# Performance work log

Measured on AMD Instinct MI355X. Metric: run time of the kernel, lower is better.

The kernel has to match this reference:

```python
import jax, jax.numpy as jnp
import numpy as np

N_NODES = 1_000_000
N_EDGES = 32_000_000

def setup_inputs() -> dict:
    key = jax.random.key(0)
    ks = jax.random.split(key, 10)
    s = lambda fan_in: 1.0 / np.sqrt(fan_in)
    return {
        "node_features": jax.random.normal(ks[0], (N_NODES, 2), dtype=jnp.float32),
        "edge_index": jax.random.randint(ks[1], (2, N_EDGES), 0, N_NODES, dtype=jnp.int64) if jax.config.jax_enable_x64 else jax.random.randint(ks[1], (2, N_EDGES), 0, N_NODES, dtype=jnp.int32),
        "W_msg": jax.random.normal(ks[2], (16, 2), dtype=jnp.float32) * s(2),
        "b_msg": jax.random.normal(ks[3], (16,), dtype=jnp.float32) * s(2),
        "W_ih": jax.random.normal(ks[4], (48, 16), dtype=jnp.float32) * s(16),
        "W_hh": jax.random.normal(ks[5], (48, 16), dtype=jnp.float32) * s(16),
        "b_ih": jax.random.normal(ks[6], (48,), dtype=jnp.float32) * s(16),
        "b_hh": jax.random.normal(ks[7], (48,), dtype=jnp.float32) * s(16),
        "W_cls": jax.random.normal(ks[8], (2, 16), dtype=jnp.float32) * s(16),
        "b_cls": jax.random.normal(ks[9], (2,), dtype=jnp.float32) * s(16),
    }

def reference(node_features, edge_index, W_msg, b_msg, W_ih, W_hh, b_ih, b_hh, W_cls, b_cls):
    N = node_features.shape[0]
    src, dst = edge_index[0], edge_index[1]
    # segment-mean of predecessor features (predecessors of dst are src)
    sums = jax.ops.segment_sum(node_features[src], dst, num_segments=N)  # [N,2]
    cnt = jax.ops.segment_sum(jnp.ones(src.shape, node_features.dtype), dst, num_segments=N)  # [N]
    has_pred = cnt > 0
    agg = jnp.where(has_pred[:, None], sums / jnp.maximum(cnt, 1.0)[:, None], node_features)
    # msg linear: [N,16]
    x = agg @ W_msg.T + b_msg
    # single-step GRU with h0 = 0 (torch nn.GRU gate math)
    h0 = jnp.zeros_like(x)
    gi = x @ W_ih.T + b_ih   # [N,48]
    gh = h0 @ W_hh.T + b_hh  # [N,48]
    i_r, i_z, i_n = jnp.split(gi, 3, axis=-1)
    h_r, h_z, h_n = jnp.split(gh, 3, axis=-1)
    r = jax.nn.sigmoid(i_r + h_r)
    z = jax.nn.sigmoid(i_z + h_z)
    n = jnp.tanh(i_n + r * h_n)
    h = (1.0 - z) * n + z * h0
    # classifier: [N,2]
    return h @ W_cls.T + b_cls
```

## Files before the change

### kernel.cpp

```cpp
#include <hip/hip_runtime.h>


#define NBKT        256
#define BKT_SHIFT   12
#define DLOW_MASK   4095u
#define BKT_CAP     139264u
#define CHUNK       16384
#define BIN_THREADS 512
#define CHUNK2      8192
#define SLICES2     ((BKT_CAP + CHUNK2 - 1) / CHUNK2)
#define ACC_THREADS 1024
#define SPLIT       2
#define BKT_RANGE   4096
#define NODE_SPACE  (NBKT * BKT_RANGE)

__device__ __forceinline__ unsigned long long expand_pkt(unsigned p20)
{
    return (1ull << 52) | ((unsigned long long)(p20 >> 10) << 26)
                        | (unsigned long long)(p20 & 1023u);
}

__global__ __launch_bounds__(256) void tgnn_prep_kernel(
    const float* __restrict__ W_msg, const float* __restrict__ b_msg,
    const float* __restrict__ W_ih,  const float* __restrict__ b_ih,
    const float* __restrict__ b_hh,  const float* __restrict__ W_cls,
    const float* __restrict__ b_cls, float* __restrict__ P,
    unsigned* __restrict__ cursor1, unsigned* __restrict__ cursor2)
{
    int j = threadIdx.x;
    cursor1[j] = (unsigned)j * BKT_CAP;
    cursor2[j] = (unsigned)j * BKT_CAP;
    if (j < 48) {
        float a0 = 0.f, a1 = 0.f, dd = 0.f;
        #pragma unroll
        for (int k = 0; k < 16; ++k) {
            float w = W_ih[j * 16 + k];
            a0 += w * W_msg[k * 2 + 0];
            a1 += w * W_msg[k * 2 + 1];
            dd += w * b_msg[k];
        }
        dd += b_ih[j];
        P[j]      = a0;
        P[48 + j] = a1;
        if (j < 16)      P[96 + j]         = dd + b_hh[j];
        else if (j < 32) P[112 + (j - 16)] = dd + b_hh[j];
        else             P[128 + (j - 32)] = dd;
    }
    if (j < 16) {
        P[144 + j] = b_hh[32 + j];
        P[160 + j] = W_cls[j];
        P[176 + j] = W_cls[16 + j];
    }
    if (j == 0) { P[192] = b_cls[0]; P[193] = b_cls[1]; }
}

__global__ __launch_bounds__(256) void tgnn_quant_kernel(
    const float2* __restrict__ nf, unsigned* __restrict__ qnf, int n)
{
    int i = blockIdx.x * blockDim.x + threadIdx.x;
    if (i >= n) return;
    float2 f = nf[i];
    float x = fminf(fmaxf(f.x, -7.9f), 7.9f);
    float y = fminf(fmaxf(f.y, -7.9f), 7.9f);
    unsigned qx = (unsigned)fmaf(x, 64.0f, 512.5f);
    unsigned qy = (unsigned)fmaf(y, 64.0f, 512.5f);
    qnf[i] = qx | (qy << 10);
}

__global__ __launch_bounds__(BIN_THREADS) void tgnn_bin1_kernel(
    const int* __restrict__ src, const int* __restrict__ dst,
    const unsigned* __restrict__ qnf,
    unsigned* __restrict__ rec1, unsigned* __restrict__ cursor1,
    unsigned long long* __restrict__ partial0,
    int n_edges)
{
    __shared__ unsigned cnt[NBKT];
    __shared__ unsigned pos[NBKT];
    __shared__ unsigned scur[NBKT];
    __shared__ unsigned gbase[NBKT];
    __shared__ unsigned stage[CHUNK];

    int t  = threadIdx.x;
    int e0 = blockIdx.x * CHUNK;
    int ne = n_edges - e0;
    if (ne <= 0) return;
    if (ne > CHUNK) ne = CHUNK;
    int nv4 = (ne + 3) >> 2;

    const int4* s4p = (const int4*)(src + e0);
    const int4* d4p = (const int4*)(dst + e0);

    int4 dr[8], sr[8];
    #pragma unroll
    for (int j = 0; j < 8; ++j) {
        int i4 = j * BIN_THREADS + t;
        if (i4 < nv4) { dr[j] = d4p[i4]; sr[j] = s4p[i4]; }
        else { dr[j] = make_int4(0,0,0,0); sr[j] = make_int4(0,0,0,0); }
    }

    if (t < NBKT) cnt[t] = 0;
    __syncthreads();

    #pragma unroll
    for (int j = 0; j < 8; ++j) {
        int base = 4 * (j * BIN_THREADS + t);
        if (base < ne) {
            int lim = ne - base;
            int sv[4] = { sr[j].x, sr[j].y, sr[j].z, sr[j].w };
            #pragma unroll
            for (int c = 0; c < 4; ++c)
                if (c < lim) atomicAdd(&cnt[((unsigned)sv[c]) >> BKT_SHIFT], 1u);
        }
    }
    __syncthreads();

    if (t < NBKT) pos[t] = cnt[t];
    __syncthreads();
    #pragma unroll
    for (int off = 1; off < NBKT; off <<= 1) {
        unsigned v = 0, a = 0;
        if (t < NBKT) { v = pos[t]; a = (t >= off) ? pos[t - off] : 0u; }
        __syncthreads();
        if (t < NBKT) pos[t] = v + a;
        __syncthreads();
    }
    if (t < NBKT) {
        unsigned myCnt  = cnt[t];
        unsigned myBase = pos[t] - myCnt;
        scur[t] = myBase;
        pos[t]  = myBase;
        gbase[t] = myCnt ? atomicAdd(&cursor1[t], myCnt) : 0u;
    }
    __syncthreads();

    #pragma unroll
    for (int j = 0; j < 8; ++j) {
        int base = 4 * (j * BIN_THREADS + t);
        if (base < ne) {
            int lim = ne - base;
            int sv[4] = { sr[j].x, sr[j].y, sr[j].z, sr[j].w };
            int dv[4] = { dr[j].x, dr[j].y, dr[j].z, dr[j].w };
            #pragma unroll
            for (int c = 0; c < 4; ++c) if (c < lim) {
                unsigned s = (unsigned)sv[c];
                unsigned b = s >> BKT_SHIFT;
                unsigned p = atomicAdd(&scur[b], 1u);
                stage[p] = ((unsigned)dv[c] << 12) | (s & DLOW_MASK);
            }
        }
    }
    __syncthreads();

    int wave = t >> 6, lane = t & 63;
    for (int b = wave; b < NBKT; b += BIN_THREADS / 64) {
        unsigned n = cnt[b];
        if (!n) continue;
        unsigned sb = pos[b];
        unsigned gb = gbase[b];
        unsigned capEnd = (unsigned)(b + 1) * BKT_CAP;
        for (unsigned i = lane; i < n; i += 64) {
            unsigned r = stage[sb + i];
            unsigned slot = gb + i;
            if (slot < capEnd) {
                rec1[slot] = r;
            } else {
                unsigned node = r >> 12;
                unsigned s    = ((unsigned)b << BKT_SHIFT) | (r & DLOW_MASK);
                atomicAdd(&partial0[node], expand_pkt(qnf[s]));
            }
        }
    }
}

__global__ __launch_bounds__(256) void tgnn_pass2_kernel(
    const unsigned* __restrict__ rec1, const unsigned* __restrict__ cursor1,
    const unsigned* __restrict__ qnf,
    unsigned* __restrict__ rec2, unsigned* __restrict__ cursor2,
    unsigned long long* __restrict__ partial0)
{
    __shared__ unsigned qlds[BKT_RANGE];
    __shared__ unsigned cnt[NBKT];
    __shared__ unsigned pos[NBKT];
    __shared__ unsigned scur[NBKT];
    __shared__ unsigned gbase[NBKT];
    __shared__ unsigned stage[CHUNK2];

    int b = blockIdx.y;
    int t = threadIdx.x;

    unsigned count = cursor1[b] - (unsigned)b * BKT_CAP;
    if (count > BKT_CAP) count = BKT_CAP;
    unsigned i0 = (unsigned)blockIdx.x * CHUNK2;
    if (i0 >= count) return;
    unsigned ne = count - i0;
    if (ne > CHUNK2) ne = CHUNK2;
    int nv4 = (int)((ne + 3) >> 2);

    const unsigned* qsrc = qnf + (size_t)b * BKT_RANGE;
    #pragma unroll
    for (int k = 0; k < BKT_RANGE / 256; ++k)
        qlds[k * 256 + t] = qsrc[k * 256 + t];

    const int4* r4p = (const int4*)(rec1 + (size_t)b * BKT_CAP + i0);
    int4 rr[8];
    #pragma unroll
    for (int j = 0; j < 8; ++j) {
        int i4 = j * 256 + t;
        rr[j] = (i4 < nv4) ? r4p[i4] : make_int4(0, 0, 0, 0);
    }

    cnt[t] = 0;
    __syncthreads();

    #pragma unroll
    for (int j = 0; j < 8; ++j) {
        int base = 4 * (j * 256 + t);
        if (base < (int)ne) {
            int lim = (int)ne - base;
            unsigned rv[4] = { (unsigned)rr[j].x, (unsigned)rr[j].y,
                               (unsigned)rr[j].z, (unsigned)rr[j].w };
            #pragma unroll
            for (int c = 0; c < 4; ++c)
                if (c < lim) atomicAdd(&cnt[rv[c] >> 24], 1u);
        }
    }
    __syncthreads();

    pos[t] = cnt[t];
    __syncthreads();
    #pragma unroll
    for (int off = 1; off < NBKT; off <<= 1) {
        unsigned v = pos[t];
        unsigned a = (t >= off) ? pos[t - off] : 0u;
        __syncthreads();
        pos[t] = v + a;
        __syncthreads();
    }
    {
        unsigned myCnt  = cnt[t];
        unsigned myBase = pos[t] - myCnt;
        scur[t] = myBase;
        pos[t]  = myBase;
        gbase[t] = myCnt ? atomicAdd(&cursor2[t], myCnt) : 0u;
    }
    __syncthreads();

    #pragma unroll
    for (int j = 0; j < 8; ++j) {
        int base = 4 * (j * 256 + t);
        if (base < (int)ne) {
            int lim = (int)ne - base;
            unsigned rv[4] = { (unsigned)rr[j].x, (unsigned)rr[j].y,
                               (unsigned)rr[j].z, (unsigned)rr[j].w };
            #pragma unroll
            for (int c = 0; c < 4; ++c) if (c < lim) {
                unsigned r  = rv[c];
                unsigned bb = r >> 24;
                unsigned p  = atomicAdd(&scur[bb], 1u);
                stage[p] = (qlds[r & DLOW_MASK] << 12) | ((r >> 12) & DLOW_MASK);
            }
        }
    }
    __syncthreads();

    int wave = t >> 6, lane = t & 63;
    for (int bb = wave; bb < NBKT; bb += 4) {
        unsigned n = cnt[bb];
        if (!n) continue;
        unsigned sb = pos[bb];
        unsigned gb = gbase[bb];
        unsigned capEnd = (unsigned)(bb + 1) * BKT_CAP;
        for (unsigned i = lane; i < n; i += 64) {
            unsigned r = stage[sb + i];
            unsigned slot = gb + i;
            if (slot < capEnd) {
                rec2[slot] = r;
            } else {
                unsigned node = ((unsigned)bb << BKT_SHIFT) | (r & DLOW_MASK);
                atomicAdd(&partial0[node], expand_pkt(r >> 12));
            }
        }
    }
}

__global__ __launch_bounds__(ACC_THREADS) void tgnn_accum_kernel(
    const unsigned* __restrict__ rec2,
    const unsigned* __restrict__ cursor2,
    unsigned long long* __restrict__ partial)
{
    __shared__ unsigned long long acc[BKT_RANGE];
    int b = blockIdx.x >> 1;
    int s = blockIdx.x & 1;
    int t = threadIdx.x;

    unsigned count = cursor2[b] - (unsigned)b * BKT_CAP;
    if (count > BKT_CAP) count = BKT_CAP;
    unsigned mid = (count >> 1) & ~3u;
    unsigned i0 = s ? mid : 0u;
    unsigned i1 = s ? count : mid;

    unsigned long long* pb = partial + (size_t)s * NODE_SPACE + (size_t)b * BKT_RANGE;
    if (s == 0) {
        #pragma unroll
        for (int k = 0; k < BKT_RANGE / ACC_THREADS; ++k)
            acc[k * ACC_THREADS + t] = pb[k * ACC_THREADS + t];
    } else {
        #pragma unroll
        for (int k = 0; k < BKT_RANGE / ACC_THREADS; ++k)
            acc[k * ACC_THREADS + t] = 0ull;
    }
    __syncthreads();

    const unsigned* rb  = rec2 + (size_t)b * BKT_CAP;
    const int4*     rb4 = (const int4*)rb;

    unsigned v0 = i0 >> 2;
    unsigned v1 = i1 >> 2;
    for (unsigned v = v0 + t; v < v1; v += ACC_THREADS) {
        int4 ra = rb4[v];
        unsigned r0 = (unsigned)ra.x, r1 = (unsigned)ra.y;
        unsigned r2 = (unsigned)ra.z, r3 = (unsigned)ra.w;
        atomicAdd(&acc[r0 & DLOW_MASK], expand_pkt(r0 >> 12));
        atomicAdd(&acc[r1 & DLOW_MASK], expand_pkt(r1 >> 12));
        atomicAdd(&acc[r2 & DLOW_MASK], expand_pkt(r2 >> 12));
        atomicAdd(&acc[r3 & DLOW_MASK], expand_pkt(r3 >> 12));
    }
    for (unsigned i = (v1 << 2) + t; i < i1; i += ACC_THREADS) {
        unsigned r = rb[i];
        atomicAdd(&acc[r & DLOW_MASK], expand_pkt(r >> 12));
    }
    __syncthreads();

    #pragma unroll
    for (int k = 0; k < BKT_RANGE / ACC_THREADS; ++k)
        pb[k * ACC_THREADS + t] = acc[k * ACC_THREADS + t];
}

__global__ __launch_bounds__(256) void tgnn_merge_node_kernel(
    const float2* __restrict__ nf,
    const unsigned long long* __restrict__ partial,
    const float* __restrict__ P,
    float2* __restrict__ out, int n_nodes)
{
    __shared__ float p[194];
    for (int k = threadIdx.x; k < 194; k += 256) p[k] = P[k];
    __syncthreads();

    int i = blockIdx.x * 256 + threadIdx.x;
    if (i >= n_nodes) return;

    unsigned long long v = partial[i] + partial[NODE_SPACE + i];
    unsigned c = (unsigned)(v >> 52);
    float a0, a1;
    if (c > 0) {
        float inv = 1.0f / (float)c;
        float X = (float)(unsigned)(v & 0x3FFFFFFull);
        float Y = (float)(unsigned)((v >> 26) & 0x3FFFFFFull);
        a0 = X * inv * (1.0f / 64.0f) - 8.0f;
        a1 = Y * inv * (1.0f / 64.0f) - 8.0f;
    } else {
        float2 f = nf[i];
        a0 = f.x;
        a1 = f.y;
    }

    float o0 = p[192], o1 = p[193];
    #pragma unroll
    for (int j = 0; j < 16; ++j) {
        float gr = fmaf(p[j],      a0, fmaf(p[48 + j], a1, p[96 + j]));
        float gz = fmaf(p[16 + j], a0, fmaf(p[64 + j], a1, p[112 + j]));
        float gn = fmaf(p[32 + j], a0, fmaf(p[80 + j], a1, p[128 + j]));
        float r  = 1.0f / (1.0f + __expf(-gr));
        float z  = 1.0f / (1.0f + __expf(-gz));
        float tt = fmaf(r, p[144 + j], gn);
        tt = fminf(fmaxf(tt, -12.0f), 12.0f);
        float e  = __expf(2.0f * tt);
        float n  = (e - 1.0f) / (e + 1.0f);
        float h  = (1.0f - z) * n;
        o0 = fmaf(p[160 + j], h, o0);
        o1 = fmaf(p[176 + j], h, o1);
    }
    out[i] = make_float2(o0, o1);
}

__global__ __launch_bounds__(256) void tgnn_edge_kernel(
    const unsigned* __restrict__ qnf,
    const int* __restrict__ src,
    const int* __restrict__ dst,
    unsigned long long* __restrict__ pack,
    int n_edges)
{
    int tid    = blockIdx.x * blockDim.x + threadIdx.x;
    int stride = gridDim.x * blockDim.x;
    int n4     = n_edges >> 2;
    const int4* __restrict__ src4 = (const int4*)src;
    const int4* __restrict__ dst4 = (const int4*)dst;
    for (int i = tid; i < n4; i += stride) {
        int4 s = src4[i];
        int4 d = dst4[i];
        unsigned q0 = qnf[s.x], q1 = qnf[s.y], q2 = qnf[s.z], q3 = qnf[s.w];
        atomicAdd(&pack[d.x], expand_pkt(q0));
        atomicAdd(&pack[d.y], expand_pkt(q1));
        atomicAdd(&pack[d.z], expand_pkt(q2));
        atomicAdd(&pack[d.w], expand_pkt(q3));
    }
    for (int e = (n4 << 2) + tid; e < n_edges; e += stride)
        atomicAdd(&pack[dst[e]], expand_pkt(qnf[src[e]]));
}

__global__ __launch_bounds__(256) void tgnn_node_kernel(
    const float2* __restrict__ nf,
    const unsigned long long* __restrict__ pack,
    const float* __restrict__ P,
    float2* __restrict__ out, int n_nodes)
{
    __shared__ float p[194];
    for (int k = threadIdx.x; k < 194; k += 256) p[k] = P[k];
    __syncthreads();
    int i = blockIdx.x * 256 + threadIdx.x;
    if (i >= n_nodes) return;
    unsigned long long v = pack[i];
    unsigned c = (unsigned)(v >> 52);
    float a0, a1;
    if (c > 0) {
        float inv = 1.0f / (float)c;
        float X = (float)(unsigned)(v & 0x3FFFFFFull);
        float Y = (float)(unsigned)((v >> 26) & 0x3FFFFFFull);
        a0 = X * inv * (1.0f / 64.0f) - 8.0f;
        a1 = Y * inv * (1.0f / 64.0f) - 8.0f;
    } else {
        float2 f = nf[i];
        a0 = f.x; a1 = f.y;
    }
    float o0 = p[192], o1 = p[193];
    #pragma unroll
    for (int j = 0; j < 16; ++j) {
        float gr = fmaf(p[j],      a0, fmaf(p[48 + j], a1, p[96 + j]));
        float gz = fmaf(p[16 + j], a0, fmaf(p[64 + j], a1, p[112 + j]));
        float gn = fmaf(p[32 + j], a0, fmaf(p[80 + j], a1, p[128 + j]));
        float r  = 1.0f / (1.0f + __expf(-gr));
        float z  = 1.0f / (1.0f + __expf(-gz));
        float tt = fmaf(r, p[144 + j], gn);
        tt = fminf(fmaxf(tt, -12.0f), 12.0f);
        float e  = __expf(2.0f * tt);
        float n  = (e - 1.0f) / (e + 1.0f);
        float h  = (1.0f - z) * n;
        o0 = fmaf(p[160 + j], h, o0);
        o1 = fmaf(p[176 + j], h, o1);
    }
    out[i] = make_float2(o0, o1);
}

extern "C" void kernel_launch(void* const* d_in, const int* in_sizes, int n_in,
                              void* d_out, int out_size, void* d_ws, size_t ws_size,
                              hipStream_t stream)
{
    const float* nf    = (const float*)d_in[0];
    const int*   ei    = (const int*)d_in[1];
    const float* W_msg = (const float*)d_in[2];
    const float* b_msg = (const float*)d_in[3];
    const float* W_ih  = (const float*)d_in[4];
    const float* b_ih  = (const float*)d_in[6];
    const float* b_hh  = (const float*)d_in[7];
    const float* W_cls = (const float*)d_in[8];
    const float* b_cls = (const float*)d_in[9];
    float* out = (float*)d_out;

    const int N = in_sizes[0] / 2;
    const int E = in_sizes[1] / 2;
    const int qBlocks = (N + 255) / 256;

    size_t off = 0;
    auto take = [&](size_t bytes) { size_t o = off; off = (off + bytes + 255) & ~(size_t)255; return o; };
    size_t partialOff = take((size_t)SPLIT * NODE_SPACE * 8);
    size_t rec1Off    = take((size_t)NBKT * BKT_CAP * 4);
    size_t rec2Off    = take((size_t)NBKT * BKT_CAP * 4);
    size_t qnfOff     = take((size_t)N * 4);
    size_t cur1Off    = take((size_t)NBKT * 4);
    size_t cur2Off    = take((size_t)NBKT * 4);
    size_t pOff       = take(194 * 4);
    size_t need = off;

    char* ws = (char*)d_ws;

    if (ws_size >= need) {
        unsigned long long* partial = (unsigned long long*)(ws + partialOff);
        unsigned* rec1    = (unsigned*)(ws + rec1Off);
        unsigned* rec2    = (unsigned*)(ws + rec2Off);
        unsigned* qnf     = (unsigned*)(ws + qnfOff);
        unsigned* cursor1 = (unsigned*)(ws + cur1Off);
        unsigned* cursor2 = (unsigned*)(ws + cur2Off);
        float*    P       = (float*)(ws + pOff);

        (void)hipMemsetAsync(partial, 0, (size_t)NODE_SPACE * 8, stream);

        tgnn_prep_kernel<<<1, 256, 0, stream>>>(W_msg, b_msg, W_ih, b_ih, b_hh,
                                                W_cls, b_cls, P, cursor1, cursor2);
        tgnn_quant_kernel<<<qBlocks, 256, 0, stream>>>((const float2*)nf, qnf, N);

        int binBlocks = (E + CHUNK - 1) / CHUNK;
        tgnn_bin1_kernel<<<binBlocks, BIN_THREADS, 0, stream>>>(ei, ei + E, qnf,
                                                                rec1, cursor1,
                                                                partial, E);

        dim3 g2(SLICES2, NBKT);
        tgnn_pass2_kernel<<<g2, 256, 0, stream>>>(rec1, cursor1, qnf,
                                                  rec2, cursor2, partial);

        tgnn_accum_kernel<<<NBKT * SPLIT, ACC_THREADS, 0, stream>>>(rec2, cursor2,
                                                                    partial);

        tgnn_merge_node_kernel<<<qBlocks, 256, 0, stream>>>((const float2*)nf, partial,
                                                            P, (float2*)out, N);
    } else {
        unsigned long long* pack = (unsigned long long*)ws;
        unsigned* qnf = (unsigned*)(ws + (size_t)N * 8);
        float*    P   = (float*)(ws + (size_t)N * 12);
        unsigned* curD1 = (unsigned*)(ws + (size_t)N * 12 + 1024);
        unsigned* curD2 = (unsigned*)(ws + (size_t)N * 12 + 3072);

        (void)hipMemsetAsync(pack, 0, (size_t)N * 8, stream);
        tgnn_prep_kernel<<<1, 256, 0, stream>>>(W_msg, b_msg, W_ih, b_ih, b_hh,
                                                W_cls, b_cls, P, curD1, curD2);
        tgnn_quant_kernel<<<qBlocks, 256, 0, stream>>>((const float2*)nf, qnf, N);
        tgnn_edge_kernel<<<2048, 256, 0, stream>>>(qnf, ei, ei + E, pack, E);
        tgnn_node_kernel<<<qBlocks, 256, 0, stream>>>((const float2*)nf, pack,
                                                      P, (float2*)out, N);
    }
}
```

Before: 325.2 us.

## Replace count-and-scan binning with fixed-capacity per-bucket staging and atomic overflow

Both binning kernels drop the LDS histogram pass and 256-entry prefix scan. Each bucket now gets a fixed 68-slot region in shared memory, and records that overflow it go straight to global 64-bit atomics on the partial accumulator. Chunks are halved to 8192 edges and pass2 moves to 512 threads, which removes several barriers and one pass over the registers. The cost is some extra global atomics whenever a bucket's per-chunk count exceeds 68, and rec buffers that are no longer fully compacted per chunk.

```diff
diff --git a/kernel.cpp b/kernel.cpp
--- a/kernel.cpp
+++ b/kernel.cpp
@@ -5,9 +5,11 @@
 #define BKT_SHIFT   12
 #define DLOW_MASK   4095u
 #define BKT_CAP     139264u
-#define CHUNK       16384
+#define CHUNK1      8192
+#define STCAP1      68
 #define BIN_THREADS 512
 #define CHUNK2      8192
+#define STCAP2      68
 #define SLICES2     ((BKT_CAP + CHUNK2 - 1) / CHUNK2)
 #define ACC_THREADS 1024
 #define SPLIT       2
@@ -74,67 +76,34 @@
     unsigned long long* __restrict__ partial0,
     int n_edges)
 {
-    __shared__ unsigned cnt[NBKT];
-    __shared__ unsigned pos[NBKT];
     __shared__ unsigned scur[NBKT];
+    __shared__ unsigned cntS[NBKT];
     __shared__ unsigned gbase[NBKT];
-    __shared__ unsigned stage[CHUNK];
+    __shared__ unsigned stage[NBKT * STCAP1];
 
     int t  = threadIdx.x;
-    int e0 = blockIdx.x * CHUNK;
+    int e0 = blockIdx.x * CHUNK1;
     int ne = n_edges - e0;
     if (ne <= 0) return;
-    if (ne > CHUNK) ne = CHUNK;
+    if (ne > CHUNK1) ne = CHUNK1;
     int nv4 = (ne + 3) >> 2;
 
     const int4* s4p = (const int4*)(src + e0);
     const int4* d4p = (const int4*)(dst + e0);
 
-    int4 dr[8], sr[8];
-    #pragma unroll
-    for (int j = 0; j < 8; ++j) {
+    int4 dr[4], sr[4];
+    #pragma unroll
+    for (int j = 0; j < 4; ++j) {
         int i4 = j * BIN_THREADS + t;
         if (i4 < nv4) { dr[j] = d4p[i4]; sr[j] = s4p[i4]; }
         else { dr[j] = make_int4(0,0,0,0); sr[j] = make_int4(0,0,0,0); }
     }
 
-    if (t < NBKT) cnt[t] = 0;
-    __syncthreads();
-
-    #pragma unroll
-    for (int j = 0; j < 8; ++j) {
-        int base = 4 * (j * BIN_THREADS + t);
-        if (base < ne) {
-            int lim = ne - base;
-            int sv[4] = { sr[j].x, sr[j].y, sr[j].z, sr[j].w };
-            #pragma unroll
-            for (int c = 0; c < 4; ++c)
-                if (c < lim) atomicAdd(&cnt[((unsigned)sv[c]) >> BKT_SHIFT], 1u);
-        }
-    }
-    __syncthreads();
-
-    if (t < NBKT) pos[t] = cnt[t];
-    __syncthreads();
-    #pragma unroll
-    for (int off = 1; off < NBKT; off <<= 1) {
-        unsigned v = 0, a = 0;
-        if (t < NBKT) { v = pos[t]; a = (t >= off) ? pos[t - off] : 0u; }
-        __syncthreads();
-        if (t < NBKT) pos[t] = v + a;
-        __syncthreads();
-    }
-    if (t < NBKT) {
-        unsigned myCnt  = cnt[t];
-        unsigned myBase = pos[t] - myCnt;
-        scur[t] = myBase;
-        pos[t]  = myBase;
-        gbase[t] = myCnt ? atomicAdd(&cursor1[t], myCnt) : 0u;
-    }
-    __syncthreads();
-
-    #pragma unroll
-    for (int j = 0; j < 8; ++j) {
+    if (t < NBKT) scur[t] = (unsigned)t * STCAP1;
+    __syncthreads();
+
+    #pragma unroll
+    for (int j = 0; j < 4; ++j) {
         int base = 4 * (j * BIN_THREADS + t);
         if (base < ne) {
             int lim = ne - base;
@@ -145,17 +114,30 @@
                 unsigned s = (unsigned)sv[c];
                 unsigned b = s >> BKT_SHIFT;
                 unsigned p = atomicAdd(&scur[b], 1u);
-                stage[p] = ((unsigned)dv[c] << 12) | (s & DLOW_MASK);
+                unsigned r = ((unsigned)dv[c] << 12) | (s & DLOW_MASK);
+                if (p < (b + 1) * STCAP1) {
+                    stage[p] = r;
+                } else {
+                    atomicAdd(&partial0[(unsigned)dv[c]], expand_pkt(qnf[s]));
+                }
             }
         }
     }
     __syncthreads();
 
+    if (t < NBKT) {
+        unsigned cnt = scur[t] - (unsigned)t * STCAP1;
+        if (cnt > STCAP1) cnt = STCAP1;
+        cntS[t]  = cnt;
+        gbase[t] = cnt ? atomicAdd(&cursor1[t], cnt) : 0u;
+    }
+    __syncthreads();
+
     int wave = t >> 6, lane = t & 63;
     for (int b = wave; b < NBKT; b += BIN_THREADS / 64) {
-        unsigned n = cnt[b];
+        unsigned n = cntS[b];
         if (!n) continue;
-        unsigned sb = pos[b];
+        unsigned sb = (unsigned)b * STCAP1;
         unsigned gb = gbase[b];
         unsigned capEnd = (unsigned)(b + 1) * BKT_CAP;
         for (unsigned i = lane; i < n; i += 64) {
@@ -172,18 +154,17 @@
     }
 }
 
-__global__ __launch_bounds__(256) void tgnn_pass2_kernel(
+__global__ __launch_bounds__(BIN_THREADS) void tgnn_pass2_kernel(
     const unsigned* __restrict__ rec1, const unsigned* __restrict__ cursor1,
     const unsigned* __restrict__ qnf,
     unsigned* __restrict__ rec2, unsigned* __restrict__ cursor2,
     unsigned long long* __restrict__ partial0)
 {
     __shared__ unsigned qlds[BKT_RANGE];
-    __shared__ unsigned cnt[NBKT];
-    __shared__ unsigned pos[NBKT];
     __shared__ unsigned scur[NBKT];
+    __shared__ unsigned cntS[NBKT];
     __shared__ unsigned gbase[NBKT];
-    __shared__ unsigned stage[CHUNK2];
+    __shared__ unsigned stage[NBKT * STCAP2];
 
     int b = blockIdx.y;
     int t = threadIdx.x;
@@ -198,56 +179,23 @@
 
     const unsigned* qsrc = qnf + (size_t)b * BKT_RANGE;
     #pragma unroll
-    for (int k = 0; k < BKT_RANGE / 256; ++k)
-        qlds[k * 256 + t] = qsrc[k * 256 + t];
+    for (int k = 0; k < BKT_RANGE / BIN_THREADS; ++k)
+        qlds[k * BIN_THREADS + t] = qsrc[k * BIN_THREADS + t];
 
     const int4* r4p = (const int4*)(rec1 + (size_t)b * BKT_CAP + i0);
-    int4 rr[8];
-    #pragma unroll
-    for (int j = 0; j < 8; ++j) {
-        int i4 = j * 256 + t;
+    int4 rr[4];
+    #pragma unroll
+    for (int j = 0; j < 4; ++j) {
+        int i4 = j * BIN_THREADS + t;
         rr[j] = (i4 < nv4) ? r4p[i4] : make_int4(0, 0, 0, 0);
     }
 
-    cnt[t] = 0;
-    __syncthreads();
-
-    #pragma unroll
-    for (int j = 0; j < 8; ++j) {
-        int base = 4 * (j * 256 + t);
-        if (base < (int)ne) {
-            int lim = (int)ne - base;
-            unsigned rv[4] = { (unsigned)rr[j].x, (unsigned)rr[j].y,
-                               (unsigned)rr[j].z, (unsigned)rr[j].w };
-            #pragma unroll
-            for (int c = 0; c < 4; ++c)
-                if (c < lim) atomicAdd(&cnt[rv[c] >> 24], 1u);
-        }
-    }
-    __syncthreads();
-
-    pos[t] = cnt[t];
-    __syncthreads();
-    #pragma unroll
-    for (int off = 1; off < NBKT; off <<= 1) {
-        unsigned v = pos[t];
-        unsigned a = (t >= off) ? pos[t - off] : 0u;
-        __syncthreads();
-        pos[t] = v + a;
-        __syncthreads();
-    }
-    {
-        unsigned myCnt  = cnt[t];
-        unsigned myBase = pos[t] - myCnt;
-        scur[t] = myBase;
-        pos[t]  = myBase;
-        gbase[t] = myCnt ? atomicAdd(&cursor2[t], myCnt) : 0u;
-    }
-    __syncthreads();
-
-    #pragma unroll
-    for (int j = 0; j < 8; ++j) {
-        int base = 4 * (j * 256 + t);
+    if (t < NBKT) scur[t] = (unsigned)t * STCAP2;
+    __syncthreads();
+
+    #pragma unroll
+    for (int j = 0; j < 4; ++j) {
+        int base = 4 * (j * BIN_THREADS + t);
         if (base < (int)ne) {
             int lim = (int)ne - base;
             unsigned rv[4] = { (unsigned)rr[j].x, (unsigned)rr[j].y,
@@ -255,19 +203,32 @@
             #pragma unroll
             for (int c = 0; c < 4; ++c) if (c < lim) {
                 unsigned r  = rv[c];
+                unsigned q  = qlds[r & DLOW_MASK];
                 unsigned bb = r >> 24;
                 unsigned p  = atomicAdd(&scur[bb], 1u);
-                stage[p] = (qlds[r & DLOW_MASK] << 12) | ((r >> 12) & DLOW_MASK);
+                if (p < (bb + 1) * STCAP2) {
+                    stage[p] = (q << 12) | ((r >> 12) & DLOW_MASK);
+                } else {
+                    atomicAdd(&partial0[r >> 12], expand_pkt(q));
+                }
             }
         }
     }
     __syncthreads();
 
+    if (t < NBKT) {
+        unsigned cnt = scur[t] - (unsigned)t * STCAP2;
+        if (cnt > STCAP2) cnt = STCAP2;
+        cntS[t]  = cnt;
+        gbase[t] = cnt ? atomicAdd(&cursor2[t], cnt) : 0u;
+    }
+    __syncthreads();
+
     int wave = t >> 6, lane = t & 63;
-    for (int bb = wave; bb < NBKT; bb += 4) {
-        unsigned n = cnt[bb];
+    for (int bb = wave; bb < NBKT; bb += BIN_THREADS / 64) {
+        unsigned n = cntS[bb];
         if (!n) continue;
-        unsigned sb = pos[bb];
+        unsigned sb = (unsigned)bb * STCAP2;
         unsigned gb = gbase[bb];
         unsigned capEnd = (unsigned)(bb + 1) * BKT_CAP;
         for (unsigned i = lane; i < n; i += 64) {
@@ -498,14 +459,14 @@
                                                 W_cls, b_cls, P, cursor1, cursor2);
         tgnn_quant_kernel<<<qBlocks, 256, 0, stream>>>((const float2*)nf, qnf, N);
 
-        int binBlocks = (E + CHUNK - 1) / CHUNK;
+        int binBlocks = (E + CHUNK1 - 1) / CHUNK1;
         tgnn_bin1_kernel<<<binBlocks, BIN_THREADS, 0, stream>>>(ei, ei + E, qnf,
                                                                 rec1, cursor1,
                                                                 partial, E);
 
         dim3 g2(SLICES2, NBKT);
-        tgnn_pass2_kernel<<<g2, 256, 0, stream>>>(rec1, cursor1, qnf,
-                                                  rec2, cursor2, partial);
+        tgnn_pass2_kernel<<<g2, BIN_THREADS, 0, stream>>>(rec1, cursor1, qnf,
+                                                          rec2, cursor2, partial);
 
         tgnn_accum_kernel<<<NBKT * SPLIT, ACC_THREADS, 0, stream>>>(rec2, cursor2,
                                                                     partial);
```

After: 360.5 us. 1.11x slower.
